# Kernel tuning notes

Hardware: AMD Instinct MI355X
Metric: run time of the kernel (lower is better)

Reference implementation:

```python
import jax, jax.numpy as jnp
import numpy as np

C = 512
NUM_HEADS = 8
HEAD_DIM = C // NUM_HEADS  # 64
BN_EPS = 1e-5


def setup_inputs() -> dict:
    key = jax.random.key(0)
    ks = jax.random.split(key, 12)
    B, H, W = 8, 32, 32
    s = 0.02
    return {
        "x": jax.random.normal(ks[0], (B, C, H, W), dtype=jnp.float32),
        "gamma": jnp.ones((C,), jnp.float32),
        "beta": jnp.zeros((C,), jnp.float32),
        "rmean": jnp.zeros((C,), jnp.float32),
        "rvar": jnp.ones((C,), jnp.float32),
        "wq": jax.random.normal(ks[1], (C, C), jnp.float32) * s,
        "bq": jnp.zeros((C,), jnp.float32),
        "wk": jax.random.normal(ks[2], (C, C), jnp.float32) * s,
        "bk": jnp.zeros((C,), jnp.float32),
        "wv": jax.random.normal(ks[3], (C, C), jnp.float32) * s,
        "bv": jnp.zeros((C,), jnp.float32),
        "wp": jax.random.normal(ks[4], (C, C), jnp.float32) * s,
        "bp": jnp.zeros((C,), jnp.float32),
    }


def _conv1x1(w, b, h):
    # 1x1 conv == per-pixel dense: (O,C) x (B,C,H,W) -> (B,O,H,W)
    return jnp.einsum('oc,bchw->bohw', w, h) + b[None, :, None, None]


def reference(x, gamma, beta, rmean, rvar, wq, bq, wk, bk, wv, bv, wp, bp):
    B, Cc, H, W = x.shape
    N = H * W
    # BatchNorm2d (eval mode, running stats)
    inv = gamma / jnp.sqrt(rvar + BN_EPS)
    h = x * inv[None, :, None, None] + (beta - rmean * inv)[None, :, None, None]
    q = _conv1x1(wq, bq, h).reshape(B, NUM_HEADS, HEAD_DIM, N)
    k = _conv1x1(wk, bk, h).reshape(B, NUM_HEADS, HEAD_DIM, N)
    v = _conv1x1(wv, bv, h).reshape(B, NUM_HEADS, HEAD_DIM, N)
    scale = 1.0 / np.sqrt(HEAD_DIM).astype(np.float32)
    attn = jnp.einsum('bhdn,bhdm->bhnm', q, k) * scale  # [B,heads,N,N]
    attn = jnp.clip(attn, -50.0, 50.0)
    attn = jax.nn.softmax(attn, axis=-1)
    out = jnp.einsum('bhnm,bhdm->bhdn', attn, v).reshape(B, Cc, H, W)
    out = _conv1x1(wp, bp, out)
    return x + out
```

## Files before the change

### kernel.cpp

```cpp
#include <hip/hip_runtime.h>
#include <stdint.h>

#define C_DIM 512
#define NHEADS 8
#define HDIM 64
#define BATCH 8
#define NPIX 1024
#define Q_PRESCALE 0.18033688011112042f

typedef __bf16 bf16x8 __attribute__((ext_vector_type(8)));
typedef float f32x4 __attribute__((ext_vector_type(4)));
typedef float f32x16 __attribute__((ext_vector_type(16)));

__device__ __forceinline__ unsigned short f2bf(float f) {
  union { float f; unsigned u; } v; v.f = f;
  unsigned r = v.u + 0x7fffu + ((v.u >> 16) & 1u);
  return (unsigned short)(r >> 16);
}

__device__ __forceinline__ void gl_lds16(const void* g, void* l) {
  __builtin_amdgcn_global_load_lds(
      (__attribute__((address_space(1))) void*)g,
      (__attribute__((address_space(3))) void*)l,
      16, 0, 0);
}

__global__ __launch_bounds__(256) void k_prep(const float* __restrict__ wq,
                                              const float* __restrict__ wk,
                                              const float* __restrict__ wv,
                                              const float* __restrict__ wp,
                                              unsigned short* __restrict__ wbf) {
  const int n = C_DIM * C_DIM;
  for (int i = blockIdx.x * blockDim.x + threadIdx.x; i < 4 * n;
       i += gridDim.x * blockDim.x) {
    const float* src = (i < n) ? wq : (i < 2 * n) ? wk : (i < 3 * n) ? wv : wp;
    wbf[i] = f2bf(src[i & (n - 1)]);
  }
}

__global__ __launch_bounds__(256) void k_bnT(const float* __restrict__ x,
                                             const float* __restrict__ gamma,
                                             const float* __restrict__ beta,
                                             const float* __restrict__ rmean,
                                             const float* __restrict__ rvar,
                                             unsigned short* __restrict__ hbT) {
  __shared__ unsigned short tile[64][72];
  const int b = blockIdx.z, c0 = blockIdx.y * 64, n0 = blockIdx.x * 64;
  const int t = threadIdx.x;
#pragma unroll
  for (int it = 0; it < 4; ++it) {
    int c = it * 16 + (t >> 4);
    int n = (t & 15) * 4;
    const float4 v = *(const float4*)&x[((size_t)b * C_DIM + c0 + c) * NPIX + n0 + n];
    int cc = c0 + c;
    float inv = gamma[cc] * rsqrtf(rvar[cc] + 1e-5f);
    float add = beta[cc] - rmean[cc] * inv;
    tile[c][n + 0] = f2bf(v.x * inv + add);
    tile[c][n + 1] = f2bf(v.y * inv + add);
    tile[c][n + 2] = f2bf(v.z * inv + add);
    tile[c][n + 3] = f2bf(v.w * inv + add);
  }
  __syncthreads();
#pragma unroll
  for (int it = 0; it < 2; ++it) {
    int n = it * 32 + (t >> 3);
    int cj = (t & 7) * 8;
    unsigned short tmp[8];
#pragma unroll
    for (int u = 0; u < 8; ++u) tmp[u] = tile[cj + u][n];
    uint4 pk;
    pk.x = (unsigned)tmp[0] | ((unsigned)tmp[1] << 16);
    pk.y = (unsigned)tmp[2] | ((unsigned)tmp[3] << 16);
    pk.z = (unsigned)tmp[4] | ((unsigned)tmp[5] << 16);
    pk.w = (unsigned)tmp[6] | ((unsigned)tmp[7] << 16);
    *(uint4*)&hbT[((size_t)b * NPIX + n0 + n) * C_DIM + c0 + cj] = pk;
  }
}

__global__ __launch_bounds__(256) void k_qkv(const unsigned short* __restrict__ wbf,
                                             const float* __restrict__ bq,
                                             const float* __restrict__ bk,
                                             const float* __restrict__ bv,
                                             const unsigned short* __restrict__ hbT,
                                             unsigned short* __restrict__ QT,
                                             unsigned short* __restrict__ KT,
                                             unsigned short* __restrict__ Vb) {
  __shared__ unsigned short Atile[128 * 64];
  __shared__ unsigned short Btile[128 * 64];
  const int which = blockIdx.z >> 3;
  const int b = blockIdx.z & 7;
  const int m0 = blockIdx.y * 128, n0 = blockIdx.x * 128;
  const unsigned short* W = wbf + (size_t)which * C_DIM * C_DIM;
  const int t = threadIdx.x, wave = t >> 6, lane = t & 63;
  const int wr = wave >> 1, wc = wave & 1;
  f32x4 acc[4][4] = {};

  for (int k0 = 0; k0 < C_DIM; k0 += 64) {
    __syncthreads();
#pragma unroll
    for (int s = 0; s < 4; ++s) {
      int row = s * 32 + wave * 8 + (lane >> 3);
      int srcc = ((lane & 7) ^ (row & 7)) * 8;
      gl_lds16(&W[(size_t)(m0 + row) * C_DIM + k0 + srcc],
               &Atile[(s * 32 + wave * 8) * 64]);
      gl_lds16(&hbT[((size_t)b * NPIX + n0 + row) * C_DIM + k0 + srcc],
               &Btile[(s * 32 + wave * 8) * 64]);
    }
    __syncthreads();
#pragma unroll
    for (int ks2 = 0; ks2 < 2; ++ks2) {
      bf16x8 af[4], bfr[4];
#pragma unroll
      for (int i = 0; i < 4; ++i) {
        int row = wr * 64 + i * 16 + (lane & 15);
        int phys = (ks2 * 4 + (lane >> 4)) ^ (row & 7);
        af[i] = *(const bf16x8*)&Atile[row * 64 + phys * 8];
      }
#pragma unroll
      for (int j = 0; j < 4; ++j) {
        int row = wc * 64 + j * 16 + (lane & 15);
        int phys = (ks2 * 4 + (lane >> 4)) ^ (row & 7);
        bfr[j] = *(const bf16x8*)&Btile[row * 64 + phys * 8];
      }
#pragma unroll
      for (int i = 0; i < 4; ++i)
#pragma unroll
        for (int j = 0; j < 4; ++j)
          acc[i][j] = __builtin_amdgcn_mfma_f32_16x16x32_bf16(af[i], bfr[j], acc[i][j], 0, 0, 0);
    }
  }

  const float* bias = (which == 0) ? bq : (which == 1) ? bk : bv;
  if (which < 2) {
    unsigned short* T = (which == 0) ? QT : KT;
    const float qs = (which == 0) ? Q_PRESCALE : 1.0f;
#pragma unroll
    for (int i = 0; i < 4; ++i) {
      int o = m0 + wr * 64 + i * 16 + (lane >> 4) * 4;
      float b0 = bias[o + 0], b1 = bias[o + 1], b2 = bias[o + 2], b3 = bias[o + 3];
#pragma unroll
      for (int j = 0; j < 4; ++j) {
        int n = n0 + wc * 64 + j * 16 + (lane & 15);
        ushort4 pk;
        pk.x = f2bf((acc[i][j][0] + b0) * qs);
        pk.y = f2bf((acc[i][j][1] + b1) * qs);
        pk.z = f2bf((acc[i][j][2] + b2) * qs);
        pk.w = f2bf((acc[i][j][3] + b3) * qs);
        *(ushort4*)&T[((size_t)b * NPIX + n) * C_DIM + o] = pk;
      }
    }
  } else {
#pragma unroll
    for (int i = 0; i < 4; ++i) {
      int o = m0 + wr * 64 + i * 16 + (lane >> 4) * 4;
#pragma unroll
      for (int j = 0; j < 4; ++j) {
        int n = n0 + wc * 64 + j * 16 + (lane & 15);
#pragma unroll
        for (int r = 0; r < 4; ++r)
          Vb[((size_t)b * C_DIM + o + r) * NPIX + n] = f2bf(acc[i][j][r] + bias[o + r]);
      }
    }
  }
}

__global__ __launch_bounds__(256) void k_attn(const unsigned short* __restrict__ QT,
                                              const unsigned short* __restrict__ KT,
                                              const unsigned short* __restrict__ Vb,
                                              unsigned short* __restrict__ OA,
                                              unsigned short* __restrict__ OB,
                                              float* __restrict__ rs) {
  __shared__ unsigned short Ks[3][64 * 64];
  __shared__ unsigned short Vs[3][64 * 64];

  const int bid = blockIdx.x;
  const int b = bid & 7, h = (bid >> 3) & 7, qt = (bid >> 6) & 7, ks = bid >> 9;
  const int n0 = qt * 128;
  const int kbase0 = ks * 512;
  const int lane = threadIdx.x & 63, wave = threadIdx.x >> 6;
  const int l31 = lane & 31, hi = lane >> 5;

  bf16x8 qf[4];
  {
    const unsigned short* qbase =
        QT + ((size_t)b * NPIX + n0 + wave * 32 + l31) * C_DIM + h * HDIM + hi * 8;
#pragma unroll
    for (int kk = 0; kk < 4; ++kk) qf[kk] = *(const bf16x8*)(qbase + kk * 16);
  }

  union { unsigned u[4]; bf16x8 v; } ones;
  ones.u[0] = 0x3F803F80u; ones.u[1] = 0x3F803F80u;
  ones.u[2] = 0x3F803F80u; ones.u[3] = 0x3F803F80u;

  auto stage = [&](int buf, int tile) {
    const int m0 = kbase0 + tile * 64;
#pragma unroll
    for (int it = 0; it < 2; ++it) {
      int rb = it * 32 + wave * 8;
      int row = rb + (lane >> 3);
      int srcc = ((lane & 7) ^ (row & 7)) * 8;
      gl_lds16(&KT[((size_t)b * NPIX + m0 + row) * C_DIM + h * HDIM + srcc],
               &Ks[buf][rb * 64]);
      gl_lds16(&Vb[((size_t)b * C_DIM + h * HDIM + row) * NPIX + m0 + srcc],
               &Vs[buf][rb * 64]);
    }
  };

  f32x16 oacc[2] = {};
  f32x16 rsacc = {};

  stage(0, 0);
  stage(1, 1);
  asm volatile("s_waitcnt vmcnt(4)" ::: "memory");
  __builtin_amdgcn_s_barrier();
  __builtin_amdgcn_sched_barrier(0);

#pragma unroll
  for (int tile = 0; tile < 8; ++tile) {
    const int cur = tile % 3;
    if (tile < 6) stage((tile + 2) % 3, tile + 2);

#pragma unroll
    for (int kt = 0; kt < 2; ++kt) {
      f32x16 s = {};
#pragma unroll
      for (int kk = 0; kk < 4; ++kk) {
        int row = kt * 32 + l31;
        int phys = (kk * 2 + hi) ^ (row & 7);
        bf16x8 kf = *(const bf16x8*)&Ks[cur][row * 64 + phys * 8];
        s = __builtin_amdgcn_mfma_f32_32x32x16_bf16(kf, qf[kk], s, 0, 0, 0);
      }
      unsigned w[8];
#pragma unroll
      for (int r2 = 0; r2 < 8; ++r2) {
        float e0 = exp2f(s[2 * r2]);
        float e1 = exp2f(s[2 * r2 + 1]);
        asm("v_cvt_pk_bf16_f32 %0, %1, %2" : "=v"(w[r2]) : "v"(e0), "v"(e1));
      }
      asm volatile("v_permlane32_swap_b32 %0, %1" : "+v"(w[0]), "+v"(w[2]));
      asm volatile("v_permlane32_swap_b32 %0, %1" : "+v"(w[1]), "+v"(w[3]));
      asm volatile("v_permlane32_swap_b32 %0, %1" : "+v"(w[4]), "+v"(w[6]));
      asm volatile("v_permlane32_swap_b32 %0, %1" : "+v"(w[5]), "+v"(w[7]));
      union U8 { unsigned u[4]; bf16x8 v; };
      U8 pa0, pa1;
      pa0.u[0] = w[0]; pa0.u[1] = w[1]; pa0.u[2] = w[2]; pa0.u[3] = w[3];
      pa1.u[0] = w[4]; pa1.u[1] = w[5]; pa1.u[2] = w[6]; pa1.u[3] = w[7];
      rsacc = __builtin_amdgcn_mfma_f32_32x32x16_bf16(pa0.v, ones.v, rsacc, 0, 0, 0);
      rsacc = __builtin_amdgcn_mfma_f32_32x32x16_bf16(pa1.v, ones.v, rsacc, 0, 0, 0);
#pragma unroll
      for (int dt = 0; dt < 2; ++dt) {
        int d = dt * 32 + l31;
        bf16x8 v0 = *(const bf16x8*)&Vs[cur][d * 64 + (((kt * 4 + hi) ^ (d & 7)) * 8)];
        bf16x8 v1 = *(const bf16x8*)&Vs[cur][d * 64 + (((kt * 4 + 2 + hi) ^ (d & 7)) * 8)];
        oacc[dt] = __builtin_amdgcn_mfma_f32_32x32x16_bf16(pa0.v, v0, oacc[dt], 0, 0, 0);
        oacc[dt] = __builtin_amdgcn_mfma_f32_32x32x16_bf16(pa1.v, v1, oacc[dt], 0, 0, 0);
      }
    }

    if (tile < 6) {
      asm volatile("s_waitcnt vmcnt(4)" ::: "memory");
      __builtin_amdgcn_s_barrier();
      __builtin_amdgcn_sched_barrier(0);
    } else if (tile == 6) {
      asm volatile("s_waitcnt vmcnt(0)" ::: "memory");
      __builtin_amdgcn_s_barrier();
      __builtin_amdgcn_sched_barrier(0);
    }
  }

  float inv[16];
#pragma unroll
  for (int r = 0; r < 16; ++r) inv[r] = 1.0f / rsacc[r];

  unsigned short* obuf = (ks == 0) ? OA : OB;
  __bf16* obase = (__bf16*)(obuf + ((size_t)b * NPIX + n0 + wave * 32) * C_DIM +
                            h * HDIM + l31);
#pragma unroll
  for (int dt = 0; dt < 2; ++dt)
#pragma unroll
    for (int r = 0; r < 16; ++r) {
      int q = (r & 3) + 8 * (r >> 2) + 4 * hi;
      obase[(size_t)q * C_DIM + dt * 32] = (__bf16)(oacc[dt][r] * inv[r]);
    }
  if (l31 == 0) {
    float* rbase = rs + (((size_t)ks * 8 + b) * 8 + h) * NPIX + n0 + wave * 32;
#pragma unroll
    for (int r = 0; r < 16; ++r)
      rbase[(r & 3) + 8 * (r >> 2) + 4 * hi] = rsacc[r];
  }
}

__global__ __launch_bounds__(256) void k_comb(const unsigned short* OA,
                                              const unsigned short* OB,
                                              const float* __restrict__ rs,
                                              unsigned short* AOT) {
  int i = blockIdx.x * 256 + threadIdx.x;
  int b = i >> 16;
  int rem = i & 65535;
  int n = rem >> 6;
  int c8 = rem & 63;
  int h = c8 >> 3;
  size_t off = ((size_t)b * NPIX + n) * C_DIM + c8 * 8;
  float rsA = rs[(((size_t)0 * 8 + b) * 8 + h) * NPIX + n];
  float rsB = rs[(((size_t)1 * 8 + b) * 8 + h) * NPIX + n];
  float sA = rsA / (rsA + rsB);
  float sB = 1.0f - sA;
  uint4 a = *(const uint4*)(OA + off);
  uint4 bb = *(const uint4*)(OB + off);
  const unsigned* au = (const unsigned*)&a;
  const unsigned* bu = (const unsigned*)&bb;
  uint4 o;
  unsigned* ou = (unsigned*)&o;
#pragma unroll
  for (int j = 0; j < 4; ++j) {
    float a0, a1, b0, b1;
    union { unsigned u; float f; } t;
    t.u = (au[j] & 0xFFFFu) << 16; a0 = t.f;
    t.u = au[j] & 0xFFFF0000u;     a1 = t.f;
    t.u = (bu[j] & 0xFFFFu) << 16; b0 = t.f;
    t.u = bu[j] & 0xFFFF0000u;     b1 = t.f;
    float o0 = sA * a0 + sB * b0;
    float o1 = sA * a1 + sB * b1;
    unsigned pk;
    asm("v_cvt_pk_bf16_f32 %0, %1, %2" : "=v"(pk) : "v"(o0), "v"(o1));
    ou[j] = pk;
  }
  *(uint4*)(AOT + off) = o;
}

__global__ __launch_bounds__(256) void k_proj(const unsigned short* __restrict__ Wp,
                                              const float* __restrict__ bp,
                                              const unsigned short* __restrict__ AOT,
                                              const float* __restrict__ x,
                                              float* __restrict__ out) {
  __shared__ unsigned short Atile[128 * 32];
  __shared__ unsigned short Btile[128 * 32];
  const int b = blockIdx.z;
  const int m0 = blockIdx.y * 128, n0 = blockIdx.x * 128;
  const int t = threadIdx.x, wave = t >> 6, lane = t & 63;
  const int wr = wave >> 1, wc = wave & 1;
  f32x4 acc[4][4] = {};
  const int st_row = lane >> 2;
  const int st_col = (((lane & 3) ^ ((lane >> 3) & 3))) * 8;

  for (int k0 = 0; k0 < C_DIM; k0 += 32) {
    __syncthreads();
#pragma unroll
    for (int it = 0; it < 2; ++it) {
      int q = wave + 4 * it;
      int row = q * 16 + st_row;
      gl_lds16(&Wp[(size_t)(m0 + row) * C_DIM + k0 + st_col], &Atile[q * 512]);
      gl_lds16(&AOT[((size_t)b * NPIX + n0 + row) * C_DIM + k0 + st_col], &Btile[q * 512]);
    }
    __syncthreads();
    bf16x8 af[4], bfr[4];
#pragma unroll
    for (int i = 0; i < 4; ++i) {
      int row = wr * 64 + i * 16 + (lane & 15);
      af[i] = *(const bf16x8*)&Atile[row * 32 + (((lane >> 4) ^ ((row >> 1) & 3)) * 8)];
    }
#pragma unroll
    for (int j = 0; j < 4; ++j) {
      int row = wc * 64 + j * 16 + (lane & 15);
      bfr[j] = *(const bf16x8*)&Btile[row * 32 + (((lane >> 4) ^ ((row >> 1) & 3)) * 8)];
    }
#pragma unroll
    for (int i = 0; i < 4; ++i)
#pragma unroll
      for (int j = 0; j < 4; ++j)
        acc[i][j] = __builtin_amdgcn_mfma_f32_16x16x32_bf16(af[i], bfr[j], acc[i][j], 0, 0, 0);
  }

#pragma unroll
  for (int i = 0; i < 4; ++i) {
    int o = m0 + wr * 64 + i * 16 + (lane >> 4) * 4;
    float b0 = bp[o + 0], b1 = bp[o + 1], b2 = bp[o + 2], b3 = bp[o + 3];
#pragma unroll
    for (int j = 0; j < 4; ++j) {
      int n = n0 + wc * 64 + j * 16 + (lane & 15);
      size_t base = ((size_t)b * C_DIM + o) * NPIX + n;
      out[base + 0 * NPIX] = acc[i][j][0] + b0 + x[base + 0 * NPIX];
      out[base + 1 * NPIX] = acc[i][j][1] + b1 + x[base + 1 * NPIX];
      out[base + 2 * NPIX] = acc[i][j][2] + b2 + x[base + 2 * NPIX];
      out[base + 3 * NPIX] = acc[i][j][3] + b3 + x[base + 3 * NPIX];
    }
  }
}

extern "C" void kernel_launch(void* const* d_in, const int* in_sizes, int n_in,
                              void* d_out, int out_size, void* d_ws, size_t ws_size,
                              hipStream_t stream) {
  (void)in_sizes; (void)n_in; (void)out_size; (void)ws_size;
  const float* x     = (const float*)d_in[0];
  const float* gamma = (const float*)d_in[1];
  const float* beta  = (const float*)d_in[2];
  const float* rmean = (const float*)d_in[3];
  const float* rvar  = (const float*)d_in[4];
  const float* wq    = (const float*)d_in[5];
  const float* bq    = (const float*)d_in[6];
  const float* wk    = (const float*)d_in[7];
  const float* bk    = (const float*)d_in[8];
  const float* wv    = (const float*)d_in[9];
  const float* bv    = (const float*)d_in[10];
  const float* wp    = (const float*)d_in[11];
  const float* bp    = (const float*)d_in[12];

  unsigned short* ws  = (unsigned short*)d_ws;
  const size_t WSZ    = (size_t)C_DIM * C_DIM;
  const size_t BIG    = (size_t)BATCH * NPIX * C_DIM;
  unsigned short* wbf = ws;
  unsigned short* hbT = wbf + 4 * WSZ;
  unsigned short* QT  = hbT + BIG;
  unsigned short* KT  = QT + BIG;
  unsigned short* Vb  = KT + BIG;
  unsigned short* AOT = Vb + BIG;
  float*          rs  = (float*)(AOT + BIG);

  k_prep<<<dim3(512), dim3(256), 0, stream>>>(wq, wk, wv, wp, wbf);
  k_bnT<<<dim3(16, 8, 8), dim3(256), 0, stream>>>(x, gamma, beta, rmean, rvar, hbT);
  k_qkv<<<dim3(8, 4, 24), dim3(256), 0, stream>>>(wbf, bq, bk, bv, hbT, QT, KT, Vb);
  k_attn<<<dim3(1024), dim3(256), 0, stream>>>(QT, KT, Vb, AOT, hbT, rs);
  k_comb<<<dim3(2048), dim3(256), 0, stream>>>(AOT, hbT, rs, AOT);
  k_proj<<<dim3(8, 4, 8), dim3(256), 0, stream>>>(wbf + 3 * WSZ, bp, AOT, x, (float*)d_out);
}
```

Measured before the change: 173.1 us.

## Split attention keys four ways with single-buffered tiles and VALU row sums

Attention work is split across four key chunks instead of two, doubling the grid to 2048 blocks. The triple-buffered asynchronous LDS pipeline becomes a single buffer with plain __syncthreads, with launch bounds requesting 6 blocks per SIMD for higher occupancy. Softmax row sums now accumulate in fp32 on the VALU plus a cross-half shuffle, replacing the extra MFMAs against a ones vector. The combine kernel merges four bf16 partials, which adds global memory traffic and drops the load/compute overlap the previous pipeline provided.

```diff
diff --git a/kernel.cpp b/kernel.cpp
--- a/kernel.cpp
+++ b/kernel.cpp
@@ -164,19 +164,19 @@
   }
 }
 
-__global__ __launch_bounds__(256) void k_attn(const unsigned short* __restrict__ QT,
-                                              const unsigned short* __restrict__ KT,
-                                              const unsigned short* __restrict__ Vb,
-                                              unsigned short* __restrict__ OA,
-                                              unsigned short* __restrict__ OB,
-                                              float* __restrict__ rs) {
-  __shared__ unsigned short Ks[3][64 * 64];
-  __shared__ unsigned short Vs[3][64 * 64];
+__global__ __launch_bounds__(256, 6) void k_attn(const unsigned short* __restrict__ QT,
+                                                 const unsigned short* __restrict__ KT,
+                                                 const unsigned short* __restrict__ Vb,
+                                                 unsigned short* __restrict__ Opart,
+                                                 float* __restrict__ rs) {
+  __shared__ unsigned short Ks[64 * 64];
+  __shared__ unsigned short Vs[64 * 64];
+  __shared__ float rs_lds[128];
 
   const int bid = blockIdx.x;
   const int b = bid & 7, h = (bid >> 3) & 7, qt = (bid >> 6) & 7, ks = bid >> 9;
   const int n0 = qt * 128;
-  const int kbase0 = ks * 512;
+  const int kbase0 = ks * 256;
   const int lane = threadIdx.x & 63, wave = threadIdx.x >> 6;
   const int l31 = lane & 31, hi = lane >> 5;
 
@@ -188,11 +188,10 @@
     for (int kk = 0; kk < 4; ++kk) qf[kk] = *(const bf16x8*)(qbase + kk * 16);
   }
 
-  union { unsigned u[4]; bf16x8 v; } ones;
-  ones.u[0] = 0x3F803F80u; ones.u[1] = 0x3F803F80u;
-  ones.u[2] = 0x3F803F80u; ones.u[3] = 0x3F803F80u;
-
-  auto stage = [&](int buf, int tile) {
+  f32x16 oacc[2] = {};
+  float rs0 = 0.f, rs1 = 0.f;
+
+  for (int tile = 0; tile < 4; ++tile) {
     const int m0 = kbase0 + tile * 64;
 #pragma unroll
     for (int it = 0; it < 2; ++it) {
@@ -200,25 +199,11 @@
       int row = rb + (lane >> 3);
       int srcc = ((lane & 7) ^ (row & 7)) * 8;
       gl_lds16(&KT[((size_t)b * NPIX + m0 + row) * C_DIM + h * HDIM + srcc],
-               &Ks[buf][rb * 64]);
+               &Ks[rb * 64]);
       gl_lds16(&Vb[((size_t)b * C_DIM + h * HDIM + row) * NPIX + m0 + srcc],
-               &Vs[buf][rb * 64]);
-    }
-  };
-
-  f32x16 oacc[2] = {};
-  f32x16 rsacc = {};
-
-  stage(0, 0);
-  stage(1, 1);
-  asm volatile("s_waitcnt vmcnt(4)" ::: "memory");
-  __builtin_amdgcn_s_barrier();
-  __builtin_amdgcn_sched_barrier(0);
-
-#pragma unroll
-  for (int tile = 0; tile < 8; ++tile) {
-    const int cur = tile % 3;
-    if (tile < 6) stage((tile + 2) % 3, tile + 2);
+               &Vs[rb * 64]);
+    }
+    __syncthreads();
 
 #pragma unroll
     for (int kt = 0; kt < 2; ++kt) {
@@ -227,7 +212,7 @@
       for (int kk = 0; kk < 4; ++kk) {
         int row = kt * 32 + l31;
         int phys = (kk * 2 + hi) ^ (row & 7);
-        bf16x8 kf = *(const bf16x8*)&Ks[cur][row * 64 + phys * 8];
+        bf16x8 kf = *(const bf16x8*)&Ks[row * 64 + phys * 8];
         s = __builtin_amdgcn_mfma_f32_32x32x16_bf16(kf, qf[kk], s, 0, 0, 0);
       }
       unsigned w[8];
@@ -235,6 +220,8 @@
       for (int r2 = 0; r2 < 8; ++r2) {
         float e0 = exp2f(s[2 * r2]);
         float e1 = exp2f(s[2 * r2 + 1]);
+        rs0 += e0;
+        rs1 += e1;
         asm("v_cvt_pk_bf16_f32 %0, %1, %2" : "=v"(w[r2]) : "v"(e0), "v"(e1));
       }
       asm volatile("v_permlane32_swap_b32 %0, %1" : "+v"(w[0]), "+v"(w[2]));
@@ -245,35 +232,30 @@
       U8 pa0, pa1;
       pa0.u[0] = w[0]; pa0.u[1] = w[1]; pa0.u[2] = w[2]; pa0.u[3] = w[3];
       pa1.u[0] = w[4]; pa1.u[1] = w[5]; pa1.u[2] = w[6]; pa1.u[3] = w[7];
-      rsacc = __builtin_amdgcn_mfma_f32_32x32x16_bf16(pa0.v, ones.v, rsacc, 0, 0, 0);
-      rsacc = __builtin_amdgcn_mfma_f32_32x32x16_bf16(pa1.v, ones.v, rsacc, 0, 0, 0);
 #pragma unroll
       for (int dt = 0; dt < 2; ++dt) {
         int d = dt * 32 + l31;
-        bf16x8 v0 = *(const bf16x8*)&Vs[cur][d * 64 + (((kt * 4 + hi) ^ (d & 7)) * 8)];
-        bf16x8 v1 = *(const bf16x8*)&Vs[cur][d * 64 + (((kt * 4 + 2 + hi) ^ (d & 7)) * 8)];
+        bf16x8 v0 = *(const bf16x8*)&Vs[d * 64 + (((kt * 4 + hi) ^ (d & 7)) * 8)];
+        bf16x8 v1 = *(const bf16x8*)&Vs[d * 64 + (((kt * 4 + 2 + hi) ^ (d & 7)) * 8)];
         oacc[dt] = __builtin_amdgcn_mfma_f32_32x32x16_bf16(pa0.v, v0, oacc[dt], 0, 0, 0);
         oacc[dt] = __builtin_amdgcn_mfma_f32_32x32x16_bf16(pa1.v, v1, oacc[dt], 0, 0, 0);
       }
     }
-
-    if (tile < 6) {
-      asm volatile("s_waitcnt vmcnt(4)" ::: "memory");
-      __builtin_amdgcn_s_barrier();
-      __builtin_amdgcn_sched_barrier(0);
-    } else if (tile == 6) {
-      asm volatile("s_waitcnt vmcnt(0)" ::: "memory");
-      __builtin_amdgcn_s_barrier();
-      __builtin_amdgcn_sched_barrier(0);
-    }
-  }
+    __syncthreads();
+  }
+
+  float rsq = rs0 + rs1;
+  rsq += __shfl_xor(rsq, 32);
+  if (hi == 0) rs_lds[wave * 32 + l31] = rsq;
+  __syncthreads();
 
   float inv[16];
 #pragma unroll
-  for (int r = 0; r < 16; ++r) inv[r] = 1.0f / rsacc[r];
-
-  unsigned short* obuf = (ks == 0) ? OA : OB;
-  __bf16* obase = (__bf16*)(obuf + ((size_t)b * NPIX + n0 + wave * 32) * C_DIM +
+  for (int r = 0; r < 16; ++r)
+    inv[r] = 1.0f / rs_lds[wave * 32 + (r & 3) + 8 * (r >> 2) + 4 * hi];
+
+  __bf16* obase = (__bf16*)(Opart + (size_t)ks * BATCH * NPIX * C_DIM +
+                            ((size_t)b * NPIX + n0 + wave * 32) * C_DIM +
                             h * HDIM + l31);
 #pragma unroll
   for (int dt = 0; dt < 2; ++dt)
@@ -282,18 +264,14 @@
       int q = (r & 3) + 8 * (r >> 2) + 4 * hi;
       obase[(size_t)q * C_DIM + dt * 32] = (__bf16)(oacc[dt][r] * inv[r]);
     }
-  if (l31 == 0) {
-    float* rbase = rs + (((size_t)ks * 8 + b) * 8 + h) * NPIX + n0 + wave * 32;
-#pragma unroll
-    for (int r = 0; r < 16; ++r)
-      rbase[(r & 3) + 8 * (r >> 2) + 4 * hi] = rsacc[r];
-  }
-}
-
-__global__ __launch_bounds__(256) void k_comb(const unsigned short* OA,
-                                              const unsigned short* OB,
+  if (hi == 0)
+    rs[(((size_t)ks * 8 + b) * 8 + h) * NPIX + n0 + wave * 32 + l31] = rsq;
+}
+
+__global__ __launch_bounds__(256) void k_comb(const unsigned short* __restrict__ Op,
                                               const float* __restrict__ rs,
-                                              unsigned short* AOT) {
+                                              unsigned short* __restrict__ AOT) {
+  const size_t BIG = (size_t)BATCH * NPIX * C_DIM;
   int i = blockIdx.x * 256 + threadIdx.x;
   int b = i >> 16;
   int rem = i & 65535;
@@ -301,28 +279,31 @@
   int c8 = rem & 63;
   int h = c8 >> 3;
   size_t off = ((size_t)b * NPIX + n) * C_DIM + c8 * 8;
-  float rsA = rs[(((size_t)0 * 8 + b) * 8 + h) * NPIX + n];
-  float rsB = rs[(((size_t)1 * 8 + b) * 8 + h) * NPIX + n];
-  float sA = rsA / (rsA + rsB);
-  float sB = 1.0f - sA;
-  uint4 a = *(const uint4*)(OA + off);
-  uint4 bb = *(const uint4*)(OB + off);
-  const unsigned* au = (const unsigned*)&a;
-  const unsigned* bu = (const unsigned*)&bb;
+  float r[4], tot = 0.f;
+#pragma unroll
+  for (int ks = 0; ks < 4; ++ks) {
+    r[ks] = rs[(((size_t)ks * 8 + b) * 8 + h) * NPIX + n];
+    tot += r[ks];
+  }
+  float itot = 1.0f / tot;
+  uint4 av[4];
+#pragma unroll
+  for (int ks = 0; ks < 4; ++ks) av[ks] = *(const uint4*)(Op + ks * BIG + off);
   uint4 o;
   unsigned* ou = (unsigned*)&o;
 #pragma unroll
   for (int j = 0; j < 4; ++j) {
-    float a0, a1, b0, b1;
-    union { unsigned u; float f; } t;
-    t.u = (au[j] & 0xFFFFu) << 16; a0 = t.f;
-    t.u = au[j] & 0xFFFF0000u;     a1 = t.f;
-    t.u = (bu[j] & 0xFFFFu) << 16; b0 = t.f;
-    t.u = bu[j] & 0xFFFF0000u;     b1 = t.f;
-    float o0 = sA * a0 + sB * b0;
-    float o1 = sA * a1 + sB * b1;
+    float lo = 0.f, hif = 0.f;
+#pragma unroll
+    for (int ks = 0; ks < 4; ++ks) {
+      unsigned u = ((const unsigned*)&av[ks])[j];
+      union { unsigned u; float f; } t;
+      float wk = r[ks] * itot;
+      t.u = (u & 0xFFFFu) << 16; lo += wk * t.f;
+      t.u = u & 0xFFFF0000u;     hif += wk * t.f;
+    }
     unsigned pk;
-    asm("v_cvt_pk_bf16_f32 %0, %1, %2" : "=v"(pk) : "v"(o0), "v"(o1));
+    asm("v_cvt_pk_bf16_f32 %0, %1, %2" : "=v"(pk) : "v"(lo), "v"(hif));
     ou[j] = pk;
   }
   *(uint4*)(AOT + off) = o;
@@ -408,18 +389,19 @@
   unsigned short* ws  = (unsigned short*)d_ws;
   const size_t WSZ    = (size_t)C_DIM * C_DIM;
   const size_t BIG    = (size_t)BATCH * NPIX * C_DIM;
-  unsigned short* wbf = ws;
-  unsigned short* hbT = wbf + 4 * WSZ;
-  unsigned short* QT  = hbT + BIG;
-  unsigned short* KT  = QT + BIG;
-  unsigned short* Vb  = KT + BIG;
-  unsigned short* AOT = Vb + BIG;
-  float*          rs  = (float*)(AOT + BIG);
+  unsigned short* wbf  = ws;
+  unsigned short* hbT  = wbf + 4 * WSZ;
+  unsigned short* QT   = hbT + BIG;
+  unsigned short* KT   = QT + BIG;
+  unsigned short* Vb   = KT + BIG;
+  unsigned short* AOT  = Vb + BIG;
+  unsigned short* Opart = AOT + BIG;
+  float*          rs   = (float*)(Opart + 4 * BIG);
 
   k_prep<<<dim3(512), dim3(256), 0, stream>>>(wq, wk, wv, wp, wbf);
   k_bnT<<<dim3(16, 8, 8), dim3(256), 0, stream>>>(x, gamma, beta, rmean, rvar, hbT);
   k_qkv<<<dim3(8, 4, 24), dim3(256), 0, stream>>>(wbf, bq, bk, bv, hbT, QT, KT, Vb);
-  k_attn<<<dim3(1024), dim3(256), 0, stream>>>(QT, KT, Vb, AOT, hbT, rs);
-  k_comb<<<dim3(2048), dim3(256), 0, stream>>>(AOT, hbT, rs, AOT);
+  k_attn<<<dim3(2048), dim3(256), 0, stream>>>(QT, KT, Vb, Opart, rs);
+  k_comb<<<dim3(2048), dim3(256), 0, stream>>>(Opart, rs, AOT);
   k_proj<<<dim3(8, 4, 8), dim3(256), 0, stream>>>(wbf + 3 * WSZ, bp, AOT, x, (float*)d_out);
 }
```

Measured after the change: 229.9 us. 32.8% more time.

## Use 512-thread attention blocks with shared K/V tiles and scalar row sums

Applied to the files above, without the earlier changes.

The attention kernel now runs 8 waves per block covering 256 query rows, so each staged K/V tile is shared by twice as many queries. Staging drops from a triple buffer with explicit vmcnt waits to a double buffer with plain __syncthreads. Row sums are now accumulated with scalar adds plus a cross-lane shuffle instead of extra MFMAs against a ones vector. Split outputs go to a separate Opart buffer so k_comb no longer reads and writes through hbT and AOT, at the cost of more workspace, fewer blocks and less load/compute overlap.

```diff
diff --git a/kernel.cpp b/kernel.cpp
--- a/kernel.cpp
+++ b/kernel.cpp
@@ -164,18 +164,18 @@
   }
 }
 
-__global__ __launch_bounds__(256) void k_attn(const unsigned short* __restrict__ QT,
-                                              const unsigned short* __restrict__ KT,
-                                              const unsigned short* __restrict__ Vb,
-                                              unsigned short* __restrict__ OA,
-                                              unsigned short* __restrict__ OB,
-                                              float* __restrict__ rs) {
-  __shared__ unsigned short Ks[3][64 * 64];
-  __shared__ unsigned short Vs[3][64 * 64];
+__global__ __launch_bounds__(512, 6) void k_attn(const unsigned short* __restrict__ QT,
+                                                 const unsigned short* __restrict__ KT,
+                                                 const unsigned short* __restrict__ Vb,
+                                                 unsigned short* __restrict__ Opart,
+                                                 float* __restrict__ rs) {
+  __shared__ unsigned short Ks[2][64 * 64];
+  __shared__ unsigned short Vs[2][64 * 64];
+  __shared__ float rs_lds[256];
 
   const int bid = blockIdx.x;
-  const int b = bid & 7, h = (bid >> 3) & 7, qt = (bid >> 6) & 7, ks = bid >> 9;
-  const int n0 = qt * 128;
+  const int b = bid & 7, h = (bid >> 3) & 7, qt = (bid >> 6) & 3, ks = bid >> 8;
+  const int n0 = qt * 256;
   const int kbase0 = ks * 512;
   const int lane = threadIdx.x & 63, wave = threadIdx.x >> 6;
   const int l31 = lane & 31, hi = lane >> 5;
@@ -188,37 +188,26 @@
     for (int kk = 0; kk < 4; ++kk) qf[kk] = *(const bf16x8*)(qbase + kk * 16);
   }
 
-  union { unsigned u[4]; bf16x8 v; } ones;
-  ones.u[0] = 0x3F803F80u; ones.u[1] = 0x3F803F80u;
-  ones.u[2] = 0x3F803F80u; ones.u[3] = 0x3F803F80u;
-
   auto stage = [&](int buf, int tile) {
     const int m0 = kbase0 + tile * 64;
-#pragma unroll
-    for (int it = 0; it < 2; ++it) {
-      int rb = it * 32 + wave * 8;
-      int row = rb + (lane >> 3);
-      int srcc = ((lane & 7) ^ (row & 7)) * 8;
-      gl_lds16(&KT[((size_t)b * NPIX + m0 + row) * C_DIM + h * HDIM + srcc],
-               &Ks[buf][rb * 64]);
-      gl_lds16(&Vb[((size_t)b * C_DIM + h * HDIM + row) * NPIX + m0 + srcc],
-               &Vs[buf][rb * 64]);
-    }
+    int rb = wave * 8;
+    int row = rb + (lane >> 3);
+    int srcc = ((lane & 7) ^ (row & 7)) * 8;
+    gl_lds16(&KT[((size_t)b * NPIX + m0 + row) * C_DIM + h * HDIM + srcc],
+             &Ks[buf][rb * 64]);
+    gl_lds16(&Vb[((size_t)b * C_DIM + h * HDIM + row) * NPIX + m0 + srcc],
+             &Vs[buf][rb * 64]);
   };
 
   f32x16 oacc[2] = {};
-  f32x16 rsacc = {};
+  float rs0 = 0.f, rs1 = 0.f;
 
   stage(0, 0);
-  stage(1, 1);
-  asm volatile("s_waitcnt vmcnt(4)" ::: "memory");
-  __builtin_amdgcn_s_barrier();
-  __builtin_amdgcn_sched_barrier(0);
-
-#pragma unroll
+  __syncthreads();
+
   for (int tile = 0; tile < 8; ++tile) {
-    const int cur = tile % 3;
-    if (tile < 6) stage((tile + 2) % 3, tile + 2);
+    const int cur = tile & 1;
+    if (tile < 7) stage(cur ^ 1, tile + 1);
 
 #pragma unroll
     for (int kt = 0; kt < 2; ++kt) {
@@ -235,6 +224,8 @@
       for (int r2 = 0; r2 < 8; ++r2) {
         float e0 = exp2f(s[2 * r2]);
         float e1 = exp2f(s[2 * r2 + 1]);
+        rs0 += e0;
+        rs1 += e1;
         asm("v_cvt_pk_bf16_f32 %0, %1, %2" : "=v"(w[r2]) : "v"(e0), "v"(e1));
       }
       asm volatile("v_permlane32_swap_b32 %0, %1" : "+v"(w[0]), "+v"(w[2]));
@@ -245,8 +236,6 @@
       U8 pa0, pa1;
       pa0.u[0] = w[0]; pa0.u[1] = w[1]; pa0.u[2] = w[2]; pa0.u[3] = w[3];
       pa1.u[0] = w[4]; pa1.u[1] = w[5]; pa1.u[2] = w[6]; pa1.u[3] = w[7];
-      rsacc = __builtin_amdgcn_mfma_f32_32x32x16_bf16(pa0.v, ones.v, rsacc, 0, 0, 0);
-      rsacc = __builtin_amdgcn_mfma_f32_32x32x16_bf16(pa1.v, ones.v, rsacc, 0, 0, 0);
 #pragma unroll
       for (int dt = 0; dt < 2; ++dt) {
         int d = dt * 32 + l31;
@@ -256,24 +245,21 @@
         oacc[dt] = __builtin_amdgcn_mfma_f32_32x32x16_bf16(pa1.v, v1, oacc[dt], 0, 0, 0);
       }
     }
-
-    if (tile < 6) {
-      asm volatile("s_waitcnt vmcnt(4)" ::: "memory");
-      __builtin_amdgcn_s_barrier();
-      __builtin_amdgcn_sched_barrier(0);
-    } else if (tile == 6) {
-      asm volatile("s_waitcnt vmcnt(0)" ::: "memory");
-      __builtin_amdgcn_s_barrier();
-      __builtin_amdgcn_sched_barrier(0);
-    }
-  }
+    __syncthreads();
+  }
+
+  float rsq = rs0 + rs1;
+  rsq += __shfl_xor(rsq, 32);
+  if (hi == 0) rs_lds[wave * 32 + l31] = rsq;
+  __syncthreads();
 
   float inv[16];
 #pragma unroll
-  for (int r = 0; r < 16; ++r) inv[r] = 1.0f / rsacc[r];
-
-  unsigned short* obuf = (ks == 0) ? OA : OB;
-  __bf16* obase = (__bf16*)(obuf + ((size_t)b * NPIX + n0 + wave * 32) * C_DIM +
+  for (int r = 0; r < 16; ++r)
+    inv[r] = 1.0f / rs_lds[wave * 32 + (r & 3) + 8 * (r >> 2) + 4 * hi];
+
+  __bf16* obase = (__bf16*)(Opart + (size_t)ks * BATCH * NPIX * C_DIM +
+                            ((size_t)b * NPIX + n0 + wave * 32) * C_DIM +
                             h * HDIM + l31);
 #pragma unroll
   for (int dt = 0; dt < 2; ++dt)
@@ -282,12 +268,8 @@
       int q = (r & 3) + 8 * (r >> 2) + 4 * hi;
       obase[(size_t)q * C_DIM + dt * 32] = (__bf16)(oacc[dt][r] * inv[r]);
     }
-  if (l31 == 0) {
-    float* rbase = rs + (((size_t)ks * 8 + b) * 8 + h) * NPIX + n0 + wave * 32;
-#pragma unroll
-    for (int r = 0; r < 16; ++r)
-      rbase[(r & 3) + 8 * (r >> 2) + 4 * hi] = rsacc[r];
-  }
+  if (hi == 0)
+    rs[(((size_t)ks * 8 + b) * 8 + h) * NPIX + n0 + wave * 32 + l31] = rsq;
 }
 
 __global__ __launch_bounds__(256) void k_comb(const unsigned short* OA,
@@ -408,18 +390,19 @@
   unsigned short* ws  = (unsigned short*)d_ws;
   const size_t WSZ    = (size_t)C_DIM * C_DIM;
   const size_t BIG    = (size_t)BATCH * NPIX * C_DIM;
-  unsigned short* wbf = ws;
-  unsigned short* hbT = wbf + 4 * WSZ;
-  unsigned short* QT  = hbT + BIG;
-  unsigned short* KT  = QT + BIG;
-  unsigned short* Vb  = KT + BIG;
-  unsigned short* AOT = Vb + BIG;
-  float*          rs  = (float*)(AOT + BIG);
+  unsigned short* wbf   = ws;
+  unsigned short* hbT   = wbf + 4 * WSZ;
+  unsigned short* QT    = hbT + BIG;
+  unsigned short* KT    = QT + BIG;
+  unsigned short* Vb    = KT + BIG;
+  unsigned short* AOT   = Vb + BIG;
+  unsigned short* Opart = AOT + BIG;
+  float*          rs    = (float*)(Opart + 2 * BIG);
 
   k_prep<<<dim3(512), dim3(256), 0, stream>>>(wq, wk, wv, wp, wbf);
   k_bnT<<<dim3(16, 8, 8), dim3(256), 0, stream>>>(x, gamma, beta, rmean, rvar, hbT);
   k_qkv<<<dim3(8, 4, 24), dim3(256), 0, stream>>>(wbf, bq, bk, bv, hbT, QT, KT, Vb);
-  k_attn<<<dim3(1024), dim3(256), 0, stream>>>(QT, KT, Vb, AOT, hbT, rs);
-  k_comb<<<dim3(2048), dim3(256), 0, stream>>>(AOT, hbT, rs, AOT);
+  k_attn<<<dim3(512), dim3(512), 0, stream>>>(QT, KT, Vb, Opart, rs);
+  k_comb<<<dim3(2048), dim3(256), 0, stream>>>(Opart, Opart + BIG, rs, AOT);
   k_proj<<<dim3(8, 4, 8), dim3(256), 0, stream>>>(wbf + 3 * WSZ, bp, AOT, x, (float*)d_out);
 }
```

Measured after the change: 203.7 us. +17.7%, slower.
